# Kernel tuning notes

Hardware: AMD Instinct MI355X
Metric: run time of the kernel (lower is better)

Reference implementation:

```python
import jax, jax.numpy as jnp
import numpy as np

NUM_USERS = 1_000_000
EMBED = 64
BATCH = 16384
DEG = 50


def setup_inputs() -> dict:
    key = jax.random.key(0)
    ks = jax.random.split(key, 7)
    return {
        "nodes": jax.random.randint(ks[0], (BATCH,), 0, NUM_USERS),
        "neighbors": jax.random.randint(ks[1], (BATCH, DEG), 0, NUM_USERS),
        "u_to_e": jax.random.normal(ks[2], (NUM_USERS, EMBED), jnp.float32) * 0.02,
        "w1": jax.random.normal(ks[3], (2 * EMBED, EMBED), jnp.float32) / np.sqrt(2 * EMBED),
        "b1": jnp.zeros((EMBED,), jnp.float32),
        "w2": jax.random.normal(ks[4], (EMBED, EMBED), jnp.float32) / np.sqrt(EMBED),
        "b2": jnp.zeros((EMBED,), jnp.float32),
        "w3": jax.random.normal(ks[5], (EMBED, 1), jnp.float32) / np.sqrt(EMBED),
        "b3": jnp.zeros((1,), jnp.float32),
    }


def reference(nodes, neighbors, u_to_e, w1, b1, w2, b2, w3, b3):
    # Gather self and neighbor embeddings
    e_u = u_to_e[nodes]            # [B, d]
    e_n = u_to_e[neighbors]        # [B, D, d]
    # GraphRec attention MLP on [neighbor_embed ; self_embed]
    x = jnp.concatenate(
        [e_n, jnp.broadcast_to(e_u[:, None, :], e_n.shape)], axis=-1
    )                              # [B, D, 2d]
    h = jax.nn.relu(x @ w1 + b1)   # [B, D, d]  (dropout is identity in eval)
    h = jax.nn.relu(h @ w2 + b2)   # [B, D, d]
    scores = (h @ w3 + b3)[..., 0] # [B, D]
    att = jax.nn.softmax(scores, axis=1)          # softmax over neighbors
    return jnp.einsum("bd,bde->be", att, e_n)      # attention-weighted neighbor sum [B, d]
```

## Files before the change

### kernel.cpp

```cpp
#include <hip/hip_runtime.h>
#include <hip/hip_bf16.h>
#include <stdint.h>


#define BATCH 16384
#define DEG 50

typedef __attribute__((ext_vector_type(8))) short short8;
typedef __attribute__((ext_vector_type(4))) float f32x4;

__device__ __forceinline__ short bf(float f) {
    __hip_bfloat16 h = __float2bfloat16(f);
    return *reinterpret_cast<short*>(&h);
}
__device__ __forceinline__ unsigned pk2(float a, float b) {
    union { unsigned u; unsigned short s[2]; } v;
    v.s[0] = (unsigned short)bf(a);
    v.s[1] = (unsigned short)bf(b);
    return v.u;
}
__device__ __forceinline__ float bf2f(short s) {
    union { float f; unsigned u; } v;
    v.u = (unsigned)(unsigned short)s << 16;
    return v.f;
}
__device__ __forceinline__ short8 cvt_row8(const float* p) {
    f32x4 a = *reinterpret_cast<const f32x4*>(p);
    f32x4 c = *reinterpret_cast<const f32x4*>(p + 4);
    union { short8 s; unsigned u[4]; } v;
    v.u[0] = pk2(a[0], a[1]); v.u[1] = pk2(a[2], a[3]);
    v.u[2] = pk2(c[0], c[1]); v.u[3] = pk2(c[2], c[3]);
    return v.s;
}

__global__ void pack_weights(const float* __restrict__ w1, const float* __restrict__ w2,
                             short8* __restrict__ ws) {
    const int f = blockIdx.x;
    const int lane = threadIdx.x;
    const int q = lane >> 4, r = lane & 15;
    const float* w = (f < 16) ? w1 : w2;
    const int g  = (f < 16) ? f : (f - 16);
    const int kt = g >> 2, t = g & 3;
    short8 s;
    #pragma unroll
    for (int j = 0; j < 8; ++j)
        s[j] = bf(w[(32*kt + 8*q + j)*64 + 16*t + r]);
    ws[f*64 + lane] = s;
}

__global__ __launch_bounds__(256, 3)
void graphrec_fused(const int* __restrict__ nodes, const int* __restrict__ neighbors,
                    const float* __restrict__ u_to_e,
                    const short8* __restrict__ wpk,
                    const float* __restrict__ b1, const float* __restrict__ b2,
                    const float* __restrict__ w3,
                    float* __restrict__ out)
{
    __shared__ short8 lds_a[24][64];
    __shared__ int    lds_nbr[4][64];
    __shared__ unsigned short lds_h1[4][1024];

    const int tid  = threadIdx.x;
    const int lane = tid & 63;
    const int wid  = tid >> 6;
    const int q    = lane >> 4;
    const int r    = lane & 15;

    #pragma unroll
    for (int i = 0; i < 6; ++i)
        reinterpret_cast<short8*>(lds_a)[tid + 256*i] = wpk[tid + 256*i];

    const int b    = blockIdx.x * 4 + wid;
    const int node = nodes[b];
    lds_nbr[wid][lane] = (lane < DEG) ? neighbors[b * DEG + lane] : 0;
    __syncthreads();

    short8 xf[4][2];
    #pragma unroll
    for (int mt = 0; mt < 4; ++mt) {
        const int nb = lds_nbr[wid][16*mt + r];
        const float* base = u_to_e + (size_t)nb * 64;
        xf[mt][0] = cvt_row8(base + 8*q);
        xf[mt][1] = cvt_row8(base + 32 + 8*q);
    }

    f32x4 cu[4];
    {
        const float* ub = u_to_e + (size_t)node * 64;
        short8 xu0 = cvt_row8(ub + 8*q);
        short8 xu1 = cvt_row8(ub + 32 + 8*q);
        #pragma unroll
        for (int t = 0; t < 4; ++t) {
            cu[t] = *reinterpret_cast<const f32x4*>(b1 + 16*t + 4*q);
            cu[t] = __builtin_amdgcn_mfma_f32_16x16x32_bf16(lds_a[8  + t][lane], xu0, cu[t], 0, 0, 0);
            cu[t] = __builtin_amdgcn_mfma_f32_16x16x32_bf16(lds_a[12 + t][lane], xu1, cu[t], 0, 0, 0);
        }
    }

    f32x4 b2v[4], w3v[4];
    #pragma unroll
    for (int t = 0; t < 4; ++t) {
        b2v[t] = *reinterpret_cast<const f32x4*>(b2 + 16*t + 4*q);
        w3v[t] = *reinterpret_cast<const f32x4*>(w3 + 16*t + 4*q);
    }

    unsigned short* h1base = lds_h1[wid];
    float agg[16];
    #pragma unroll
    for (int i = 0; i < 16; ++i) agg[i] = 0.f;
    float m_run = -INFINITY, s_run = 0.f;

    #pragma unroll
    for (int mt = 0; mt < 4; ++mt) {
        f32x4 acc[4] = { cu[0], cu[1], cu[2], cu[3] };
        #pragma unroll
        for (int kt = 0; kt < 2; ++kt)
            #pragma unroll
            for (int t = 0; t < 4; ++t)
                acc[t] = __builtin_amdgcn_mfma_f32_16x16x32_bf16(lds_a[kt*4 + t][lane], xf[mt][kt], acc[t], 0, 0, 0);

        #pragma unroll
        for (int t = 0; t < 4; ++t) {
            unsigned lo = pk2(fmaxf(acc[t][0], 0.f), fmaxf(acc[t][1], 0.f));
            unsigned hi = pk2(fmaxf(acc[t][2], 0.f), fmaxf(acc[t][3], 0.f));
            int off = r * 128 + (((16*t + 4*q) * 2) ^ ((r & 7) << 4));
            *reinterpret_cast<uint2*>((char*)h1base + off) = make_uint2(lo, hi);
        }
        f32x4 acc2[4];
        #pragma unroll
        for (int t2 = 0; t2 < 4; ++t2) acc2[t2] = (f32x4){0.f, 0.f, 0.f, 0.f};
        #pragma unroll
        for (int kt2 = 0; kt2 < 2; ++kt2) {
            int roff = r * 128 + (((32*kt2 + 8*q) * 2) ^ ((r & 7) << 4));
            short8 b2f = *reinterpret_cast<const short8*>((const char*)h1base + roff);
            #pragma unroll
            for (int t2 = 0; t2 < 4; ++t2)
                acc2[t2] = __builtin_amdgcn_mfma_f32_16x16x32_bf16(lds_a[16 + kt2*4 + t2][lane], b2f, acc2[t2], 0, 0, 0);
        }
        float sp = 0.f;
        #pragma unroll
        for (int t2 = 0; t2 < 4; ++t2)
            #pragma unroll
            for (int reg = 0; reg < 4; ++reg)
                sp += fmaxf(acc2[t2][reg] + b2v[t2][reg], 0.f) * w3v[t2][reg];
        sp += __shfl_xor(sp, 16, 64);
        sp += __shfl_xor(sp, 32, 64);

        float v = (mt < 3 || r < 2) ? sp : -INFINITY;
        float tm = v;
        tm = fmaxf(tm, __shfl_xor(tm, 1, 64));
        tm = fmaxf(tm, __shfl_xor(tm, 2, 64));
        tm = fmaxf(tm, __shfl_xor(tm, 4, 64));
        tm = fmaxf(tm, __shfl_xor(tm, 8, 64));
        float m_new = fmaxf(m_run, tm);
        float scale = __expf(m_run - m_new);
        float w = __expf(v - m_new);
        s_run = s_run * scale + w;
        #pragma unroll
        for (int kt = 0; kt < 2; ++kt)
            #pragma unroll
            for (int j = 0; j < 8; ++j)
                agg[kt*8 + j] = fmaf(agg[kt*8 + j], scale, w * bf2f(xf[mt][kt][j]));
        m_run = m_new;
    }

    float sum = s_run;
    sum += __shfl_xor(sum, 1, 64);
    sum += __shfl_xor(sum, 2, 64);
    sum += __shfl_xor(sum, 4, 64);
    sum += __shfl_xor(sum, 8, 64);
    float inv = 1.f / sum;
    #pragma unroll
    for (int i = 0; i < 16; ++i) agg[i] *= inv;
    #pragma unroll
    for (int d = 1; d < 16; d <<= 1)
        #pragma unroll
        for (int i = 0; i < 16; ++i)
            agg[i] += __shfl_xor(agg[i], d, 64);

    if (r == 0) {
        float* ob = out + (size_t)b * 64;
        f32x4 o0 = { agg[0],  agg[1],  agg[2],  agg[3]  };
        f32x4 o1 = { agg[4],  agg[5],  agg[6],  agg[7]  };
        f32x4 o2 = { agg[8],  agg[9],  agg[10], agg[11] };
        f32x4 o3 = { agg[12], agg[13], agg[14], agg[15] };
        *reinterpret_cast<f32x4*>(ob + 8*q)          = o0;
        *reinterpret_cast<f32x4*>(ob + 8*q + 4)      = o1;
        *reinterpret_cast<f32x4*>(ob + 32 + 8*q)     = o2;
        *reinterpret_cast<f32x4*>(ob + 32 + 8*q + 4) = o3;
    }
}

extern "C" void kernel_launch(void* const* d_in, const int* in_sizes, int n_in,
                              void* d_out, int out_size, void* d_ws, size_t ws_size,
                              hipStream_t stream) {
    const int*   nodes     = (const int*)d_in[0];
    const int*   neighbors = (const int*)d_in[1];
    const float* u_to_e    = (const float*)d_in[2];
    const float* w1        = (const float*)d_in[3];
    const float* b1        = (const float*)d_in[4];
    const float* w2        = (const float*)d_in[5];
    const float* b2        = (const float*)d_in[6];
    const float* w3        = (const float*)d_in[7];

    pack_weights<<<dim3(24), dim3(64), 0, stream>>>(w1, w2, (short8*)d_ws);
    graphrec_fused<<<dim3(BATCH / 4), dim3(256), 0, stream>>>(
        nodes, neighbors, u_to_e, (const short8*)d_ws, b1, b2, w3, (float*)d_out);
}
```

Baseline: 72.31 us.

## Split each batch row's neighbors across two waves with LDS softmax merge

Each batch row is now processed by two waves, each handling two of the four 16-neighbor tiles, instead of one wave per row. The partial online-softmax max, sum and weighted aggregate are merged through LDS with extra block barriers. The grid doubles and the launch-bounds occupancy hint rises from 3 to 4. The goal is more waves in flight and lower register pressure to hide gather latency. The cost is duplicated self-embedding GEMM and weight staging per block, plus extra synchronisation.

Measured after the change: 89.94 us. +24.4%, slower.

```diff
diff --git a/kernel.cpp b/kernel.cpp
--- a/kernel.cpp
+++ b/kernel.cpp
@@ -48,7 +48,7 @@
     ws[f*64 + lane] = s;
 }
 
-__global__ __launch_bounds__(256, 3)
+__global__ __launch_bounds__(256, 4)
 void graphrec_fused(const int* __restrict__ nodes, const int* __restrict__ neighbors,
                     const float* __restrict__ u_to_e,
                     const short8* __restrict__ wpk,
@@ -57,31 +57,37 @@
                     float* __restrict__ out)
 {
     __shared__ short8 lds_a[24][64];
-    __shared__ int    lds_nbr[4][64];
+    __shared__ int    lds_nbr[2][64];
     __shared__ unsigned short lds_h1[4][1024];
-
-    const int tid  = threadIdx.x;
-    const int lane = tid & 63;
-    const int wid  = tid >> 6;
-    const int q    = lane >> 4;
-    const int r    = lane & 15;
+    __shared__ float  lds_m[2][2];
+    __shared__ float  lds_s[2][2];
+    __shared__ float  lds_agg[2][2][64];
+
+    const int tid   = threadIdx.x;
+    const int lane  = tid & 63;
+    const int wid   = tid >> 6;
+    const int q     = lane >> 4;
+    const int r     = lane & 15;
+    const int nloc  = wid >> 1;
+    const int wpart = wid & 1;
 
     #pragma unroll
     for (int i = 0; i < 6; ++i)
         reinterpret_cast<short8*>(lds_a)[tid + 256*i] = wpk[tid + 256*i];
 
-    const int b    = blockIdx.x * 4 + wid;
+    const int b    = blockIdx.x * 2 + nloc;
     const int node = nodes[b];
-    lds_nbr[wid][lane] = (lane < DEG) ? neighbors[b * DEG + lane] : 0;
+    if (wpart == 0)
+        lds_nbr[nloc][lane] = (lane < DEG) ? neighbors[b * DEG + lane] : 0;
     __syncthreads();
 
-    short8 xf[4][2];
-    #pragma unroll
-    for (int mt = 0; mt < 4; ++mt) {
-        const int nb = lds_nbr[wid][16*mt + r];
+    short8 xf[2][2];
+    #pragma unroll
+    for (int mtl = 0; mtl < 2; ++mtl) {
+        const int nb = lds_nbr[nloc][16*(2*wpart + mtl) + r];
         const float* base = u_to_e + (size_t)nb * 64;
-        xf[mt][0] = cvt_row8(base + 8*q);
-        xf[mt][1] = cvt_row8(base + 32 + 8*q);
+        xf[mtl][0] = cvt_row8(base + 8*q);
+        xf[mtl][1] = cvt_row8(base + 32 + 8*q);
     }
 
     f32x4 cu[4];
@@ -111,13 +117,14 @@
     float m_run = -INFINITY, s_run = 0.f;
 
     #pragma unroll
-    for (int mt = 0; mt < 4; ++mt) {
+    for (int mtl = 0; mtl < 2; ++mtl) {
+        const int mt_g = 2*wpart + mtl;
         f32x4 acc[4] = { cu[0], cu[1], cu[2], cu[3] };
         #pragma unroll
         for (int kt = 0; kt < 2; ++kt)
             #pragma unroll
             for (int t = 0; t < 4; ++t)
-                acc[t] = __builtin_amdgcn_mfma_f32_16x16x32_bf16(lds_a[kt*4 + t][lane], xf[mt][kt], acc[t], 0, 0, 0);
+                acc[t] = __builtin_amdgcn_mfma_f32_16x16x32_bf16(lds_a[kt*4 + t][lane], xf[mtl][kt], acc[t], 0, 0, 0);
 
         #pragma unroll
         for (int t = 0; t < 4; ++t) {
@@ -146,7 +153,7 @@
         sp += __shfl_xor(sp, 16, 64);
         sp += __shfl_xor(sp, 32, 64);
 
-        float v = (mt < 3 || r < 2) ? sp : -INFINITY;
+        float v = (mt_g < 3 || r < 2) ? sp : -INFINITY;
         float tm = v;
         tm = fmaxf(tm, __shfl_xor(tm, 1, 64));
         tm = fmaxf(tm, __shfl_xor(tm, 2, 64));
@@ -160,18 +167,24 @@
         for (int kt = 0; kt < 2; ++kt)
             #pragma unroll
             for (int j = 0; j < 8; ++j)
-                agg[kt*8 + j] = fmaf(agg[kt*8 + j], scale, w * bf2f(xf[mt][kt][j]));
+                agg[kt*8 + j] = fmaf(agg[kt*8 + j], scale, w * bf2f(xf[mtl][kt][j]));
         m_run = m_new;
     }
 
-    float sum = s_run;
-    sum += __shfl_xor(sum, 1, 64);
-    sum += __shfl_xor(sum, 2, 64);
-    sum += __shfl_xor(sum, 4, 64);
-    sum += __shfl_xor(sum, 8, 64);
-    float inv = 1.f / sum;
-    #pragma unroll
-    for (int i = 0; i < 16; ++i) agg[i] *= inv;
+    if (lane == 0) lds_m[nloc][wpart] = m_run;
+    __syncthreads();
+    const float m_all = fmaxf(lds_m[nloc][0], lds_m[nloc][1]);
+    const float resc  = __expf(m_run - m_all);
+
+    float s = s_run;
+    s += __shfl_xor(s, 1, 64);
+    s += __shfl_xor(s, 2, 64);
+    s += __shfl_xor(s, 4, 64);
+    s += __shfl_xor(s, 8, 64);
+    s *= resc;
+
+    #pragma unroll
+    for (int i = 0; i < 16; ++i) agg[i] *= resc;
     #pragma unroll
     for (int d = 1; d < 16; d <<= 1)
         #pragma unroll
@@ -179,15 +192,19 @@
             agg[i] += __shfl_xor(agg[i], d, 64);
 
     if (r == 0) {
-        float* ob = out + (size_t)b * 64;
-        f32x4 o0 = { agg[0],  agg[1],  agg[2],  agg[3]  };
-        f32x4 o1 = { agg[4],  agg[5],  agg[6],  agg[7]  };
-        f32x4 o2 = { agg[8],  agg[9],  agg[10], agg[11] };
-        f32x4 o3 = { agg[12], agg[13], agg[14], agg[15] };
-        *reinterpret_cast<f32x4*>(ob + 8*q)          = o0;
-        *reinterpret_cast<f32x4*>(ob + 8*q + 4)      = o1;
-        *reinterpret_cast<f32x4*>(ob + 32 + 8*q)     = o2;
-        *reinterpret_cast<f32x4*>(ob + 32 + 8*q + 4) = o3;
+        #pragma unroll
+        for (int kt = 0; kt < 2; ++kt)
+            #pragma unroll
+            for (int j = 0; j < 8; ++j)
+                lds_agg[nloc][wpart][32*kt + 8*q + j] = agg[kt*8 + j];
+        if (lane == 0) lds_s[nloc][wpart] = s;
+    }
+    __syncthreads();
+
+    if (wpart == 0) {
+        float num = lds_agg[nloc][0][lane] + lds_agg[nloc][1][lane];
+        float inv = 1.f / (lds_s[nloc][0] + lds_s[nloc][1]);
+        out[(size_t)b * 64 + lane] = num * inv;
     }
 }
 
@@ -204,6 +221,6 @@
     const float* w3        = (const float*)d_in[7];
 
     pack_weights<<<dim3(24), dim3(64), 0, stream>>>(w1, w2, (short8*)d_ws);
-    graphrec_fused<<<dim3(BATCH / 4), dim3(256), 0, stream>>>(
+    graphrec_fused<<<dim3(BATCH / 2), dim3(256), 0, stream>>>(
         nodes, neighbors, u_to_e, (const short8*)d_ws, b1, b2, w3, (float*)d_out);
 }
```

## Stream neighbor embedding tiles through LDS with async global_load_lds double buffering

Applied to the files above, without the earlier changes.

Neighbor embedding rows are no longer loaded into registers up front. They are streamed per 16-row tile into a per-wave double-buffered LDS staging area using global_load_lds, with the next tiles issued while the current tile's MLP runs, and vmcnt waits gate each tile. This is meant to cut register pressure and overlap the random-row gather with MFMA work. It adds 32KB of LDS per block and lowers the launch-bounds occupancy hint from 3 to 2, which may reduce the number of resident blocks.

Result: no change. 73.75 us (+2.0%).

```diff
diff --git a/kernel.cpp b/kernel.cpp
--- a/kernel.cpp
+++ b/kernel.cpp
@@ -24,13 +24,16 @@
     v.u = (unsigned)(unsigned short)s << 16;
     return v.f;
 }
-__device__ __forceinline__ short8 cvt_row8(const float* p) {
-    f32x4 a = *reinterpret_cast<const f32x4*>(p);
-    f32x4 c = *reinterpret_cast<const f32x4*>(p + 4);
+__device__ __forceinline__ short8 pkrow(f32x4 a, f32x4 c) {
     union { short8 s; unsigned u[4]; } v;
     v.u[0] = pk2(a[0], a[1]); v.u[1] = pk2(a[2], a[3]);
     v.u[2] = pk2(c[0], c[1]); v.u[3] = pk2(c[2], c[3]);
     return v.s;
+}
+__device__ __forceinline__ short8 cvt_row8(const float* p) {
+    f32x4 a = *reinterpret_cast<const f32x4*>(p);
+    f32x4 c = *reinterpret_cast<const f32x4*>(p + 4);
+    return pkrow(a, c);
 }
 
 __global__ void pack_weights(const float* __restrict__ w1, const float* __restrict__ w2,
@@ -48,7 +51,7 @@
     ws[f*64 + lane] = s;
 }
 
-__global__ __launch_bounds__(256, 3)
+__global__ __launch_bounds__(256, 2)
 void graphrec_fused(const int* __restrict__ nodes, const int* __restrict__ neighbors,
                     const float* __restrict__ u_to_e,
                     const short8* __restrict__ wpk,
@@ -59,6 +62,7 @@
     __shared__ short8 lds_a[24][64];
     __shared__ int    lds_nbr[4][64];
     __shared__ unsigned short lds_h1[4][1024];
+    __shared__ float  lds_stage[4][2][1024];
 
     const int tid  = threadIdx.x;
     const int lane = tid & 63;
@@ -75,14 +79,9 @@
     lds_nbr[wid][lane] = (lane < DEG) ? neighbors[b * DEG + lane] : 0;
     __syncthreads();
 
-    short8 xf[4][2];
-    #pragma unroll
-    for (int mt = 0; mt < 4; ++mt) {
-        const int nb = lds_nbr[wid][16*mt + r];
-        const float* base = u_to_e + (size_t)nb * 64;
-        xf[mt][0] = cvt_row8(base + 8*q);
-        xf[mt][1] = cvt_row8(base + 32 + 8*q);
-    }
+    int rowv[4];
+    #pragma unroll
+    for (int mt = 0; mt < 4; ++mt) rowv[mt] = lds_nbr[wid][16*mt + r];
 
     f32x4 cu[4];
     {
@@ -96,7 +95,6 @@
             cu[t] = __builtin_amdgcn_mfma_f32_16x16x32_bf16(lds_a[12 + t][lane], xu1, cu[t], 0, 0, 0);
         }
     }
-
     f32x4 b2v[4], w3v[4];
     #pragma unroll
     for (int t = 0; t < 4; ++t) {
@@ -104,6 +102,22 @@
         w3v[t] = *reinterpret_cast<const f32x4*>(w3 + 16*t + 4*q);
     }
 
+    float* stg = &lds_stage[wid][0][0];
+    #define ISSUE_TILE(MT) do {                                                          \
+        const float* base_ = u_to_e + (size_t)rowv[MT] * 64 + 4*q;                       \
+        float* dst_ = stg + ((MT) & 1) * 1024;                                           \
+        _Pragma("unroll")                                                                \
+        for (int c_ = 0; c_ < 4; ++c_)                                                   \
+            __builtin_amdgcn_global_load_lds(                                            \
+                (const __attribute__((address_space(1))) void*)(base_ + 16*c_),         \
+                (__attribute__((address_space(3))) void*)(dst_ + 256*c_), 16, 0, 0);    \
+    } while (0)
+
+    __builtin_amdgcn_sched_barrier(0);
+    ISSUE_TILE(0);
+    ISSUE_TILE(1);
+    __builtin_amdgcn_sched_barrier(0);
+
     unsigned short* h1base = lds_h1[wid];
     float agg[16];
     #pragma unroll
@@ -112,12 +126,27 @@
 
     #pragma unroll
     for (int mt = 0; mt < 4; ++mt) {
+        if (mt < 3) asm volatile("s_waitcnt vmcnt(4)" ::: "memory");
+        else        asm volatile("s_waitcnt vmcnt(0)" ::: "memory");
+        __builtin_amdgcn_sched_barrier(0);
+
+        const float* bp  = stg + (mt & 1) * 1024;
+        const int boff   = (q >> 1) * 256 + (q & 1) * 128 + 4*r;
+        f32x4 A  = *reinterpret_cast<const f32x4*>(bp + boff);
+        f32x4 Bv = *reinterpret_cast<const f32x4*>(bp + boff + 64);
+        f32x4 C  = *reinterpret_cast<const f32x4*>(bp + boff + 512);
+        f32x4 Dv = *reinterpret_cast<const f32x4*>(bp + boff + 576);
+        short8 xf0 = pkrow(A, Bv);
+        short8 xf1 = pkrow(C, Dv);
+
+        if (mt < 2) ISSUE_TILE(mt + 2);
+
         f32x4 acc[4] = { cu[0], cu[1], cu[2], cu[3] };
         #pragma unroll
-        for (int kt = 0; kt < 2; ++kt)
-            #pragma unroll
-            for (int t = 0; t < 4; ++t)
-                acc[t] = __builtin_amdgcn_mfma_f32_16x16x32_bf16(lds_a[kt*4 + t][lane], xf[mt][kt], acc[t], 0, 0, 0);
+        for (int t = 0; t < 4; ++t) {
+            acc[t] = __builtin_amdgcn_mfma_f32_16x16x32_bf16(lds_a[t][lane],     xf0, acc[t], 0, 0, 0);
+            acc[t] = __builtin_amdgcn_mfma_f32_16x16x32_bf16(lds_a[4 + t][lane], xf1, acc[t], 0, 0, 0);
+        }
 
         #pragma unroll
         for (int t = 0; t < 4; ++t) {
@@ -159,10 +188,13 @@
         #pragma unroll
         for (int kt = 0; kt < 2; ++kt)
             #pragma unroll
-            for (int j = 0; j < 8; ++j)
-                agg[kt*8 + j] = fmaf(agg[kt*8 + j], scale, w * bf2f(xf[mt][kt][j]));
+            for (int j = 0; j < 8; ++j) {
+                float e = bf2f((kt == 0) ? xf0[j] : xf1[j]);
+                agg[kt*8 + j] = fmaf(agg[kt*8 + j], scale, w * e);
+            }
         m_run = m_new;
     }
+    #undef ISSUE_TILE
 
     float sum = s_run;
     sum += __shfl_xor(sum, 1, 64);
@@ -180,14 +212,10 @@
 
     if (r == 0) {
         float* ob = out + (size_t)b * 64;
-        f32x4 o0 = { agg[0],  agg[1],  agg[2],  agg[3]  };
-        f32x4 o1 = { agg[4],  agg[5],  agg[6],  agg[7]  };
-        f32x4 o2 = { agg[8],  agg[9],  agg[10], agg[11] };
-        f32x4 o3 = { agg[12], agg[13], agg[14], agg[15] };
-        *reinterpret_cast<f32x4*>(ob + 8*q)          = o0;
-        *reinterpret_cast<f32x4*>(ob + 8*q + 4)      = o1;
-        *reinterpret_cast<f32x4*>(ob + 32 + 8*q)     = o2;
-        *reinterpret_cast<f32x4*>(ob + 32 + 8*q + 4) = o3;
+        *reinterpret_cast<f32x4*>(ob + 8*q)          = (f32x4){ agg[0],  agg[1],  agg[2],  agg[3]  };
+        *reinterpret_cast<f32x4*>(ob + 8*q + 4)      = (f32x4){ agg[4],  agg[5],  agg[6],  agg[7]  };
+        *reinterpret_cast<f32x4*>(ob + 32 + 8*q)     = (f32x4){ agg[8],  agg[9],  agg[10], agg[11] };
+        *reinterpret_cast<f32x4*>(ob + 32 + 8*q + 4) = (f32x4){ agg[12], agg[13], agg[14], agg[15] };
     }
 }
 
```
